# Performance work log

Measured on AMD Instinct MI355X. Metric: run time of the kernel, lower is better.

Reference implementation:

```python
import jax, jax.numpy as jnp
import numpy as np

D, H, KVH, HD, FF = 768, 12, 4, 64, 2048
N_REP = H // KVH
EPS = 1e-6


def rmsnorm(x, w):
    # Faithful to source: norm = ||x|| * n^{-1/2}; eps added to norm (not inside sqrt)
    norm = jnp.sqrt(jnp.sum(x * x, axis=-1, keepdims=True)) * (x.shape[-1] ** -0.5)
    return w * x / (norm + EPS)


def rope_tables(seq_len, head_dim, base=10000.0):
    inv_freq = 1.0 / (base ** (np.arange(0, head_dim, 2, dtype=np.float32) / head_dim))
    t = np.arange(seq_len, dtype=np.float32)
    freqs = np.einsum('i,j->ij', t, inv_freq)  # [S, HD/2]
    emb = np.concatenate([freqs, freqs], axis=-1)  # [S, HD]
    return jnp.asarray(np.cos(emb)), jnp.asarray(np.sin(emb))


def rotate_half(x):
    h = x.shape[-1] // 2
    return jnp.concatenate([-x[..., h:], x[..., :h]], axis=-1)


def setup_inputs() -> dict:
    key = jax.random.key(0)
    ks = jax.random.split(key, 9)
    s = 0.02
    return {
        'x': jax.random.normal(ks[0], (2, 2048, D), jnp.float32),
        'Wq': jax.random.normal(ks[1], (H * HD, D), jnp.float32) * s,
        'Wk': jax.random.normal(ks[2], (KVH * HD, D), jnp.float32) * s,
        'Wv': jax.random.normal(ks[3], (KVH * HD, D), jnp.float32) * s,
        'Wo': jax.random.normal(ks[4], (D, H * HD), jnp.float32) * s,
        'Wgate': jax.random.normal(ks[5], (FF, D), jnp.float32) * s,
        'Wup': jax.random.normal(ks[6], (FF, D), jnp.float32) * s,
        'Wdown': jax.random.normal(ks[7], (D, FF), jnp.float32) * s,
        'g1': jnp.ones((D,), jnp.float32),
        'g2': jnp.ones((D,), jnp.float32),
    }


def reference(x, Wq, Wk, Wv, Wo, Wgate, Wup, Wdown, g1, g2):
    B, S, _ = x.shape
    # ---- attention sublayer (pre-norm) ----
    xn = rmsnorm(x, g1)
    q = (xn @ Wq.T).reshape(B, S, H, HD).transpose(0, 2, 1, 3)      # [B,H,S,HD]
    k = (xn @ Wk.T).reshape(B, S, KVH, HD).transpose(0, 2, 1, 3)    # [B,KVH,S,HD]
    v = (xn @ Wv.T).reshape(B, S, KVH, HD).transpose(0, 2, 1, 3)
    cos, sin = rope_tables(S, HD)                                   # [S,HD]
    q = q * cos + rotate_half(q) * sin
    k = k * cos + rotate_half(k) * sin
    # repeat kv heads to match q heads
    k = jnp.repeat(k, N_REP, axis=1)                                # [B,H,S,HD]
    v = jnp.repeat(v, N_REP, axis=1)
    scores = jnp.einsum('bhqd,bhkd->bhqk', q, k) / jnp.sqrt(jnp.float32(HD))
    causal = jnp.tril(jnp.ones((S, S), bool))
    scores = jnp.where(causal, scores, jnp.finfo(scores.dtype).min)
    attn = jax.nn.softmax(scores, axis=-1)
    out = jnp.einsum('bhqk,bhkd->bhqd', attn, v)                    # [B,H,S,HD]
    out = out.transpose(0, 2, 1, 3).reshape(B, S, H * HD) @ Wo.T
    x = x + out
    # ---- SwiGLU FFN sublayer (pre-norm) ----
    xn2 = rmsnorm(x, g2)
    ff = (jax.nn.silu(xn2 @ Wgate.T) * (xn2 @ Wup.T)) @ Wdown.T
    return x + ff
```

## Files before the change

kernel.cpp:

```cpp
#include <hip/hip_runtime.h>
#include <hip/hip_bf16.h>
#include <math.h>

typedef __bf16 bf16;
typedef __attribute__((ext_vector_type(8))) __bf16 bf16x8;
typedef __attribute__((ext_vector_type(4))) __bf16 bf16x4;
typedef __attribute__((ext_vector_type(4))) float f32x4;

#define MFMA16(a,b,c) __builtin_amdgcn_mfma_f32_16x16x32_bf16(a,b,c,0,0,0)

#define BATCH 2
#define SEQ   2048
#define DMODEL 768
#define NH    12
#define NKV   4
#define NREP  3
#define HD    64
#define FFDIM 2048
#define ROWS  (BATCH*SEQ)

#define QSCALE 0.18033688011112042f
#define LOG2E  1.4426950408889634f

#define WB(N) asm volatile("s_waitcnt vmcnt(" #N ")\n\ts_barrier" ::: "memory")
#define BAR() asm volatile("s_barrier" ::: "memory")

__device__ __forceinline__ void gl2lds16(const bf16* g, bf16* l) {
  __builtin_amdgcn_global_load_lds(
      (const __attribute__((address_space(1))) void*)g,
      (__attribute__((address_space(3))) void*)l, 16, 0, 0);
}

#define SRC_SWZ(tt)  ((((tt) & 3) ^ (((tt) >> 3) & 3)) * 8)
#define RD_SWZ(l15,lq) (((lq) ^ (((l15) >> 1) & 3)) * 8)

struct Cvt7 { const float* s[7]; bf16* d[7]; int n[7]; };
__global__ __launch_bounds__(256) void cvt_all_kernel(Cvt7 c) {
  int seg = blockIdx.y;
  const float* __restrict__ src = c.s[seg];
  bf16* __restrict__ dst = c.d[seg];
  int n = c.n[seg];
  int stride = gridDim.x * 256;
  for (int i = blockIdx.x * 256 + threadIdx.x; i < n; i += stride)
    dst[i] = (bf16)src[i];
}

__global__ __launch_bounds__(256) void rope_tab_kernel(float* __restrict__ tab) {
  int id = blockIdx.x * 256 + threadIdx.x;
  int j = id >> 11, s = id & 2047;
  float inv = expf(-(float)j * (9.210340371976184f / 32.0f));
  float ang = (float)s * inv;
  tab[id] = cosf(ang);
  tab[65536 + id] = sinf(ang);
}

__global__ __launch_bounds__(192) void rmsnorm_kernel(const float* __restrict__ x,
    const float* __restrict__ g, bf16* __restrict__ out) {
  int row = blockIdx.x;
  const float* xr = x + (size_t)row * DMODEL;
  int t = threadIdx.x;
  f32x4 v = *(const f32x4*)(xr + t * 4);
  float ss = v[0] * v[0] + v[1] * v[1] + v[2] * v[2] + v[3] * v[3];
  #pragma unroll
  for (int off = 32; off; off >>= 1) ss += __shfl_xor(ss, off, 64);
  __shared__ float red[3];
  if ((t & 63) == 0) red[t >> 6] = ss;
  __syncthreads();
  float total = red[0] + red[1] + red[2];
  float norm = sqrtf(total) * 0.03608439182435161f;
  float sc = 1.0f / (norm + 1e-6f);
  f32x4 gv = *(const f32x4*)(g + t * 4);
  bf16x4 o;
  #pragma unroll
  for (int i = 0; i < 4; ++i) o[i] = (bf16)(gv[i] * v[i] * sc);
  *(bf16x4*)(out + (size_t)row * DMODEL + t * 4) = o;
}

__global__ __launch_bounds__(512, 6) void gemm_out_kernel(const bf16* __restrict__ A,
    const bf16* __restrict__ B, float* __restrict__ C, const float* __restrict__ R,
    int N, int K) {
  __shared__ __align__(16) bf16 At[2][3][64 * 32];
  __shared__ __align__(16) bf16 Bt[2][3][64 * 32];
  int t = threadIdx.x;
  int g = t >> 8;
  int tt = t & 255;
  int lane = t & 63;
  int w = (t >> 6) & 3;
  int l15 = lane & 15, lq = lane >> 4;
  int wrow = (w >> 1) * 32, wcol = (w & 1) * 32;
  int sw = RD_SWZ(l15, lq);

  int flat = blockIdx.y * 12 + blockIdx.x;
  int f2 = (flat & 7) * 96 + (flat >> 3);
  int col0 = (f2 % 12) * 64, row0 = (f2 / 12) * 64;

  const int KH = K >> 1;
  const int NS = KH / 32;
  int scol = SRC_SWZ(tt);
  const bf16* Ag = A + (size_t)(row0 + (tt >> 2)) * K + g * KH + scol;
  const bf16* Bg = B + (size_t)(col0 + (tt >> 2)) * K + g * KH + scol;

  #pragma unroll
  for (int s = 0; s < 3; ++s) {
    gl2lds16(Ag + s * 32, At[g][s] + tt * 8);
    gl2lds16(Bg + s * 32, Bt[g][s] + tt * 8);
  }

  f32x4 zero = {0.f, 0.f, 0.f, 0.f};
  f32x4 acc[2][2];
  #pragma unroll
  for (int m = 0; m < 2; ++m)
    #pragma unroll
    for (int n = 0; n < 2; ++n) acc[m][n] = zero;

  #define OG_COMPUTE(slot) do {                                              \
    const bf16* at = At[g][slot]; const bf16* bt = Bt[g][slot];              \
    bf16x8 af[2], bb[2];                                                     \
    _Pragma("unroll")                                                        \
    for (int m = 0; m < 2; ++m)                                              \
      af[m] = *(const bf16x8*)(at + (wrow + m * 16 + l15) * 32 + sw);        \
    _Pragma("unroll")                                                        \
    for (int n = 0; n < 2; ++n)                                              \
      bb[n] = *(const bf16x8*)(bt + (wcol + n * 16 + l15) * 32 + sw);        \
    _Pragma("unroll")                                                        \
    for (int m = 0; m < 2; ++m)                                              \
      _Pragma("unroll")                                                      \
      for (int n = 0; n < 2; ++n)                                            \
        acc[m][n] = MFMA16(af[m], bb[n], acc[m][n]);                         \
  } while (0)

  int slot = 0;
  for (int k = 0; k < NS - 2; ++k) {
    WB(4);
    OG_COMPUTE(slot);
    BAR();
    if (k <= NS - 4) {
      int ks = (k + 3) * 32;
      gl2lds16(Ag + ks, At[g][slot] + tt * 8);
      gl2lds16(Bg + ks, Bt[g][slot] + tt * 8);
    }
    slot = (slot == 2) ? 0 : slot + 1;
  }
  for (int k = NS - 2; k < NS; ++k) {
    WB(0);
    OG_COMPUTE(slot);
    slot = (slot == 2) ? 0 : slot + 1;
  }
  #undef OG_COMPUTE

  __syncthreads();
  float* Cl = (float*)&At[0][0][0];
  if (g == 1) {
    #pragma unroll
    for (int m = 0; m < 2; ++m)
      #pragma unroll
      for (int n = 0; n < 2; ++n)
        #pragma unroll
        for (int r = 0; r < 4; ++r)
          Cl[(wrow + m * 16 + lq * 4 + r) * 64 + wcol + n * 16 + l15] = acc[m][n][r];
  }
  __syncthreads();
  if (g == 0) {
    #pragma unroll
    for (int m = 0; m < 2; ++m)
      #pragma unroll
      for (int n = 0; n < 2; ++n)
        #pragma unroll
        for (int r = 0; r < 4; ++r) {
          int row = wrow + m * 16 + lq * 4 + r;
          int col = wcol + n * 16 + l15;
          size_t idx = (size_t)(row0 + row) * N + col0 + col;
          C[idx] = acc[m][n][r] + Cl[row * 64 + col] + R[idx];
        }
  }
}

__global__ __launch_bounds__(256) void gemm_qkv_kernel(const bf16* __restrict__ A,
    const bf16* __restrict__ Wcat, const float* __restrict__ tab,
    bf16* __restrict__ Qh, bf16* __restrict__ Kh, bf16* __restrict__ Vt) {
  __shared__ __align__(16) bf16 At[4][64 * 32];
  __shared__ __align__(16) bf16 Bt[4][128 * 32];
  const int K = DMODEL;
  int t = threadIdx.x, lane = t & 63, wave = t >> 6;
  int l15 = lane & 15, lq = lane >> 4;
  int wrow = (wave >> 1) * 32, wcol = (wave & 1) * 64;
  int sw = RD_SWZ(l15, lq);
  int row0 = blockIdx.y * 64, col0 = blockIdx.x * 128;
  int scol = SRC_SWZ(t);
  const bf16* Ag  = A + (size_t)(row0 + (t >> 2)) * K + scol;
  const bf16* Bg0 = Wcat + (size_t)(col0 + (t >> 2)) * K + scol;
  const bf16* Bg1 = Bg0 + (size_t)64 * K;
  const int NS = K / 32;

  #pragma unroll
  for (int s = 0; s < 4; ++s) {
    int ks = s * 32;
    gl2lds16(Ag + ks,  At[s] + t * 8);
    gl2lds16(Bg0 + ks, Bt[s] + t * 8);
    gl2lds16(Bg1 + ks, Bt[s] + 2048 + t * 8);
  }

  f32x4 zero = {0.f, 0.f, 0.f, 0.f};
  f32x4 acc[2][4];
  #pragma unroll
  for (int m = 0; m < 2; ++m)
    #pragma unroll
    for (int n = 0; n < 4; ++n) acc[m][n] = zero;

  #define QK_COMPUTE(slot) do {                                              \
    const bf16* at = At[slot]; const bf16* bt = Bt[slot];                    \
    bf16x8 af[2], bfr[4];                                                    \
    _Pragma("unroll")                                                        \
    for (int m = 0; m < 2; ++m)                                              \
      af[m] = *(const bf16x8*)(at + (wrow + m * 16 + l15) * 32 + sw);        \
    _Pragma("unroll")                                                        \
    for (int n = 0; n < 4; ++n)                                              \
      bfr[n] = *(const bf16x8*)(bt + (wcol + n * 16 + l15) * 32 + sw);       \
    _Pragma("unroll")                                                        \
    for (int m = 0; m < 2; ++m)                                              \
      _Pragma("unroll")                                                      \
      for (int n = 0; n < 4; ++n)                                            \
        acc[m][n] = MFMA16(af[m], bfr[n], acc[m][n]);                        \
  } while (0)

  for (int k = 0; k < NS - 3; ++k) {
    WB(9);
    QK_COMPUTE(k & 3);
    BAR();
    if (k <= NS - 5) {
      int ks = (k + 4) * 32;
      gl2lds16(Ag + ks,  At[k & 3] + t * 8);
      gl2lds16(Bg0 + ks, Bt[k & 3] + t * 8);
      gl2lds16(Bg1 + ks, Bt[k & 3] + 2048 + t * 8);
    }
  }
  for (int k = NS - 3; k < NS; ++k) {
    WB(0);
    QK_COMPUTE(k & 3);
  }
  #undef QK_COMPUTE

  int b = row0 >> 11;
  int s0 = (row0 & 2047) + wrow + lq * 4;
  int colw = col0 + wcol;
  if (colw < 768) {
    int h = colw >> 6;
    f32x4 cv[2][2], sv[2][2];
    #pragma unroll
    for (int m = 0; m < 2; ++m)
      #pragma unroll
      for (int jh = 0; jh < 2; ++jh) {
        const float* cp = tab + (jh * 16 + l15) * 2048 + s0 + m * 16;
        cv[m][jh] = *(const f32x4*)cp;
        sv[m][jh] = *(const f32x4*)(cp + 65536);
      }
    #pragma unroll
    for (int m = 0; m < 2; ++m)
      #pragma unroll
      for (int n = 0; n < 4; ++n) {
        float sgn = (n < 2) ? -1.f : 1.f;
        #pragma unroll
        for (int r = 0; r < 4; ++r) {
          float c = cv[m][n & 1][r], si = sv[m][n & 1][r];
          float rp = (acc[m][n][r] * c + sgn * acc[m][n ^ 2][r] * si) * QSCALE;
          Qh[((size_t)(b * NH + h) * SEQ + s0 + m * 16 + r) * 64 + n * 16 + l15] = (bf16)rp;
        }
      }
  } else if (colw < 1024) {
    int kh = (colw - 768) >> 6;
    f32x4 cv[2][2], sv[2][2];
    #pragma unroll
    for (int m = 0; m < 2; ++m)
      #pragma unroll
      for (int jh = 0; jh < 2; ++jh) {
        const float* cp = tab + (jh * 16 + l15) * 2048 + s0 + m * 16;
        cv[m][jh] = *(const f32x4*)cp;
        sv[m][jh] = *(const f32x4*)(cp + 65536);
      }
    #pragma unroll
    for (int m = 0; m < 2; ++m)
      #pragma unroll
      for (int n = 0; n < 4; ++n) {
        float sgn = (n < 2) ? -1.f : 1.f;
        #pragma unroll
        for (int r = 0; r < 4; ++r) {
          float c = cv[m][n & 1][r], si = sv[m][n & 1][r];
          float rp = acc[m][n][r] * c + sgn * acc[m][n ^ 2][r] * si;
          Kh[((size_t)(b * NKV + kh) * SEQ + s0 + m * 16 + r) * 64 + n * 16 + l15] = (bf16)rp;
        }
      }
  } else {
    int vh = (colw - 1024) >> 6;
    #pragma unroll
    for (int m = 0; m < 2; ++m)
      #pragma unroll
      for (int n = 0; n < 4; ++n) {
        bf16x4 pv;
        #pragma unroll
        for (int r = 0; r < 4; ++r) pv[r] = (bf16)acc[m][n][r];
        *(bf16x4*)(Vt + ((size_t)(b * NKV + vh) * 64 + n * 16 + l15) * SEQ + s0 + m * 16) = pv;
      }
  }
}

__global__ __launch_bounds__(256) void gemm_gu_kernel(const bf16* __restrict__ A,
    const bf16* __restrict__ Wg, const bf16* __restrict__ Wu, bf16* __restrict__ H) {
  __shared__ __align__(16) bf16 At[3][128 * 32];
  __shared__ __align__(16) bf16 Bgt[3][64 * 32];
  __shared__ __align__(16) bf16 But[3][64 * 32];
  const int K = DMODEL;
  int t = threadIdx.x, lane = t & 63, wave = t >> 6;
  int l15 = lane & 15, lq = lane >> 4;
  int wrow = (wave >> 1) * 64, wcol = (wave & 1) * 32;
  int sw = RD_SWZ(l15, lq);
  int row0 = blockIdx.y * 128, col0 = blockIdx.x * 64;
  int scol = SRC_SWZ(t);
  const bf16* Ag0 = A + (size_t)(row0 + (t >> 2)) * K + scol;
  const bf16* Ag1 = Ag0 + (size_t)64 * K;
  const bf16* Gg  = Wg + (size_t)(col0 + (t >> 2)) * K + scol;
  const bf16* Ug  = Wu + (size_t)(col0 + (t >> 2)) * K + scol;
  const int NS = K / 32;

  #pragma unroll
  for (int s = 0; s < 3; ++s) {
    int ks = s * 32;
    gl2lds16(Ag0 + ks, At[s] + t * 8);
    gl2lds16(Ag1 + ks, At[s] + 2048 + t * 8);
    gl2lds16(Gg + ks,  Bgt[s] + t * 8);
    gl2lds16(Ug + ks,  But[s] + t * 8);
  }

  f32x4 zero = {0.f, 0.f, 0.f, 0.f};
  f32x4 ag[4][2], au[4][2];
  #pragma unroll
  for (int m = 0; m < 4; ++m)
    #pragma unroll
    for (int n = 0; n < 2; ++n) { ag[m][n] = zero; au[m][n] = zero; }

  #define GU_COMPUTE(slot) do {                                              \
    const bf16* at = At[slot];                                               \
    const bf16* bgt = Bgt[slot]; const bf16* but = But[slot];                \
    bf16x8 af[4], bg[2], bu[2];                                              \
    _Pragma("unroll")                                                        \
    for (int m = 0; m < 4; ++m)                                              \
      af[m] = *(const bf16x8*)(at + (wrow + m * 16 + l15) * 32 + sw);        \
    _Pragma("unroll")                                                        \
    for (int n = 0; n < 2; ++n) {                                            \
      bg[n] = *(const bf16x8*)(bgt + (wcol + n * 16 + l15) * 32 + sw);       \
      bu[n] = *(const bf16x8*)(but + (wcol + n * 16 + l15) * 32 + sw);       \
    }                                                                        \
    _Pragma("unroll")                                                        \
    for (int m = 0; m < 4; ++m)                                              \
      _Pragma("unroll")                                                      \
      for (int n = 0; n < 2; ++n) {                                          \
        ag[m][n] = MFMA16(af[m], bg[n], ag[m][n]);                           \
        au[m][n] = MFMA16(af[m], bu[n], au[m][n]);                           \
      }                                                                      \
  } while (0)

  int slot = 0;
  for (int k = 0; k < NS - 2; ++k) {
    WB(8);
    GU_COMPUTE(slot);
    BAR();
    if (k <= NS - 4) {
      int ks = (k + 3) * 32;
      gl2lds16(Ag0 + ks, At[slot] + t * 8);
      gl2lds16(Ag1 + ks, At[slot] + 2048 + t * 8);
      gl2lds16(Gg + ks,  Bgt[slot] + t * 8);
      gl2lds16(Ug + ks,  But[slot] + t * 8);
    }
    slot = (slot == 2) ? 0 : slot + 1;
  }
  for (int k = NS - 2; k < NS; ++k) {
    WB(0);
    GU_COMPUTE(slot);
    slot = (slot == 2) ? 0 : slot + 1;
  }
  #undef GU_COMPUTE

  #pragma unroll
  for (int m = 0; m < 4; ++m)
    #pragma unroll
    for (int n = 0; n < 2; ++n)
      #pragma unroll
      for (int r = 0; r < 4; ++r) {
        int row = row0 + wrow + m * 16 + lq * 4 + r;
        int col = col0 + wcol + n * 16 + l15;
        float g = ag[m][n][r], u = au[m][n][r];
        float sg = g / (1.f + __builtin_amdgcn_exp2f(-g * LOG2E));
        H[(size_t)row * FFDIM + col] = (bf16)(sg * u);
      }
}

__global__ __launch_bounds__(256) void attn_kernel(const bf16* __restrict__ Qh,
    const bf16* __restrict__ Kh, const bf16* __restrict__ Vt, bf16* __restrict__ out) {
  __shared__ __align__(16) bf16 Kl0[2][64 * 32];
  __shared__ __align__(16) bf16 Kl1[2][64 * 32];
  __shared__ __align__(16) bf16 Vl0[2][64 * 32];
  __shared__ __align__(16) bf16 Vl1[2][64 * 32];
  __shared__ __align__(16) bf16 P[4][16 * 80];

  int idx = blockIdx.x;
  int qt = 31 - (idx / 24);
  int bh = idx % 24;
  int q0blk = qt * 64;
  int b = bh / NH, h = bh % NH;
  int kvh = h / NREP;
  int t = threadIdx.x;
  int lane = t & 63, wave = t >> 6;
  int l15 = lane & 15, lq = lane >> 4;
  int qw = q0blk + wave * 16;
  const bf16* Qb = Qh + (size_t)(b * NH + h) * SEQ * 64;
  const bf16* Kb = Kh + (size_t)(b * NKV + kvh) * SEQ * 64;
  const bf16* Vb = Vt + (size_t)(b * NKV + kvh) * 64 * SEQ;

  bf16x8 bq0 = *(const bf16x8*)(Qb + (size_t)(qw + l15) * 64 + lq * 8);
  bf16x8 bq1 = *(const bf16x8*)(Qb + (size_t)(qw + l15) * 64 + 32 + lq * 8);

  const bf16* Kg = Kb + (size_t)(t >> 2) * 64 + (t & 3) * 8;
  const bf16* Vg = Vb + (size_t)(t >> 2) * SEQ + (t & 3) * 8;
  bf16* Pw = P[wave];
  int Pwq = l15 * 80, lq8 = lq * 8, lq4 = lq * 4;
  const int NS = qt + 1;

  #pragma unroll
  for (int s = 0; s < 2; ++s) {
    int ks = (s < NS ? s : NS - 1) * 64;
    gl2lds16(Kg + (size_t)ks * 64,      Kl0[s] + t * 8);
    gl2lds16(Kg + (size_t)ks * 64 + 32, Kl1[s] + t * 8);
    gl2lds16(Vg + ks,                   Vl0[s] + t * 8);
    gl2lds16(Vg + ks + 32,              Vl1[s] + t * 8);
  }

  f32x4 zero = {0.f, 0.f, 0.f, 0.f};
  f32x4 o[4];
  o[0] = zero; o[1] = zero; o[2] = zero; o[3] = zero;
  float l_r = 0.f;

  #define ATTN_STEP(kk, slot) do {                                           \
    int k0 = (kk) * 64;                                                      \
    const bf16* kl0 = Kl0[slot]; const bf16* kl1 = Kl1[slot];                \
    const bf16* vl0 = Vl0[slot]; const bf16* vl1 = Vl1[slot];                \
    f32x4 s[4];                                                              \
    _Pragma("unroll")                                                        \
    for (int c = 0; c < 4; ++c) {                                            \
      bf16x8 ak0 = *(const bf16x8*)(kl0 + (c * 16 + l15) * 32 + lq8);        \
      bf16x8 ak1 = *(const bf16x8*)(kl1 + (c * 16 + l15) * 32 + lq8);        \
      s[c] = zero;                                                           \
      s[c] = MFMA16(ak0, bq0, s[c]);                                         \
      s[c] = MFMA16(ak1, bq1, s[c]);                                         \
    }                                                                        \
    if (k0 + 63 > qw) {                                                      \
      int qmk = qw + l15 - k0 - lq4;                                         \
      _Pragma("unroll")                                                      \
      for (int c = 0; c < 4; ++c)                                            \
        _Pragma("unroll")                                                    \
        for (int r = 0; r < 4; ++r)                                          \
          if (c * 16 + r > qmk) s[c][r] = -INFINITY;                         \
    }                                                                        \
    _Pragma("unroll")                                                        \
    for (int c = 0; c < 4; ++c) {                                            \
      bf16x4 pe;                                                             \
      _Pragma("unroll")                                                      \
      for (int r = 0; r < 4; ++r) {                                          \
        float e = __builtin_amdgcn_exp2f(s[c][r]);                           \
        l_r += e;                                                            \
        pe[r] = (bf16)e;                                                     \
      }                                                                      \
      *(bf16x4*)(Pw + Pwq + c * 16 + lq4) = pe;                              \
    }                                                                        \
    bf16x8 bp0 = *(const bf16x8*)(Pw + Pwq + lq8);                           \
    bf16x8 bp1 = *(const bf16x8*)(Pw + Pwq + 32 + lq8);                      \
    _Pragma("unroll")                                                        \
    for (int n = 0; n < 4; ++n) {                                            \
      bf16x8 av0 = *(const bf16x8*)(vl0 + (n * 16 + l15) * 32 + lq8);        \
      bf16x8 av1 = *(const bf16x8*)(vl1 + (n * 16 + l15) * 32 + lq8);        \
      o[n] = MFMA16(av0, bp0, o[n]);                                         \
      o[n] = MFMA16(av1, bp1, o[n]);                                         \
    }                                                                        \
  } while (0)

  for (int k = 0; k < NS - 1; ++k) {
    WB(4);
    ATTN_STEP(k, k & 1);
    BAR();
    if (k <= NS - 3) {
      int ks = (k + 2) * 64;
      gl2lds16(Kg + (size_t)ks * 64,      Kl0[k & 1] + t * 8);
      gl2lds16(Kg + (size_t)ks * 64 + 32, Kl1[k & 1] + t * 8);
      gl2lds16(Vg + ks,                   Vl0[k & 1] + t * 8);
      gl2lds16(Vg + ks + 32,              Vl1[k & 1] + t * 8);
    }
  }
  {
    WB(0);
    ATTN_STEP(NS - 1, (NS - 1) & 1);
  }
  #undef ATTN_STEP

  float lt = l_r;
  lt += __shfl_xor(lt, 16, 64);
  lt += __shfl_xor(lt, 32, 64);
  float inv = 1.f / lt;
  int q = qw + l15;
  bf16* orow = out + (size_t)(b * SEQ + q) * DMODEL + h * 64;
  #pragma unroll
  for (int n = 0; n < 4; ++n) {
    bf16x4 po;
    #pragma unroll
    for (int r = 0; r < 4; ++r) po[r] = (bf16)(o[n][r] * inv);
    *(bf16x4*)(orow + n * 16 + lq4) = po;
  }
}

extern "C" void kernel_launch(void* const* d_in, const int* in_sizes, int n_in,
                              void* d_out, int out_size, void* d_ws, size_t ws_size,
                              hipStream_t stream) {
  const float* x     = (const float*)d_in[0];
  const float* Wq    = (const float*)d_in[1];
  const float* Wk    = (const float*)d_in[2];
  const float* Wv    = (const float*)d_in[3];
  const float* Wo    = (const float*)d_in[4];
  const float* Wgate = (const float*)d_in[5];
  const float* Wup   = (const float*)d_in[6];
  const float* Wdown = (const float*)d_in[7];
  const float* g1    = (const float*)d_in[8];
  const float* g2    = (const float*)d_in[9];
  float* out = (float*)d_out;

  char* ws = (char*)d_ws;
  size_t off = 0;
  auto alloc = [&](size_t bytes) { size_t o = off; off += (bytes + 255) & ~(size_t)255; return o; };
  size_t o_tab  = alloc((size_t)2 * 32 * 2048 * 4);
  size_t o_x1   = alloc((size_t)4096 * 768 * 4);
  size_t o_xn   = alloc((size_t)4096 * 768 * 2);
  size_t o_Qh   = alloc((size_t)2 * 12 * 2048 * 64 * 2);
  size_t o_Kh   = alloc((size_t)2 * 4 * 2048 * 64 * 2);
  size_t o_Vt   = alloc((size_t)2 * 4 * 64 * 2048 * 2);
  size_t o_ao   = alloc((size_t)4096 * 768 * 2);
  size_t o_H    = alloc((size_t)4096 * 2048 * 2);
  size_t o_Wcat = alloc((size_t)1280 * 768 * 2);
  size_t o_Wo   = alloc((size_t)768 * 768 * 2);
  size_t o_Wgu  = alloc((size_t)4096 * 768 * 2);
  size_t o_Wdn  = alloc((size_t)768 * 2048 * 2);
  if (ws_size < off) return;

  float* tab  = (float*)(ws + o_tab);
  float* fx1  = (float*)(ws + o_x1);
  bf16* bxn   = (bf16*)(ws + o_xn);
  bf16* bQh   = (bf16*)(ws + o_Qh);
  bf16* bKh   = (bf16*)(ws + o_Kh);
  bf16* bVt   = (bf16*)(ws + o_Vt);
  bf16* bao   = (bf16*)(ws + o_ao);
  bf16* bH    = (bf16*)(ws + o_H);
  bf16* bWcat = (bf16*)(ws + o_Wcat);
  bf16* bWo   = (bf16*)(ws + o_Wo);
  bf16* bWgu  = (bf16*)(ws + o_Wgu);
  bf16* bWdn  = (bf16*)(ws + o_Wdn);

  rope_tab_kernel<<<256, 256, 0, stream>>>(tab);

  Cvt7 c;
  c.s[0] = Wq;    c.d[0] = bWcat;              c.n[0] = 768 * 768;
  c.s[1] = Wk;    c.d[1] = bWcat + 768 * 768;  c.n[1] = 256 * 768;
  c.s[2] = Wv;    c.d[2] = bWcat + 1024 * 768; c.n[2] = 256 * 768;
  c.s[3] = Wo;    c.d[3] = bWo;                c.n[3] = 768 * 768;
  c.s[4] = Wgate; c.d[4] = bWgu;               c.n[4] = 2048 * 768;
  c.s[5] = Wup;   c.d[5] = bWgu + 2048 * 768;  c.n[5] = 2048 * 768;
  c.s[6] = Wdown; c.d[6] = bWdn;               c.n[6] = 768 * 2048;
  cvt_all_kernel<<<dim3(256, 7), 256, 0, stream>>>(c);

  rmsnorm_kernel<<<4096, 192, 0, stream>>>(x, g1, bxn);
  gemm_qkv_kernel<<<dim3(10, 64), 256, 0, stream>>>(bxn, bWcat, tab, bQh, bKh, bVt);
  attn_kernel<<<dim3(768), 256, 0, stream>>>(bQh, bKh, bVt, bao);
  gemm_out_kernel<<<dim3(12, 64), 512, 0, stream>>>(bao, bWo, fx1, x, 768, 768);

  rmsnorm_kernel<<<4096, 192, 0, stream>>>(fx1, g2, bxn);
  gemm_gu_kernel<<<dim3(32, 32), 256, 0, stream>>>(bxn, bWgu, bWgu + 2048 * 768, bH);
  gemm_out_kernel<<<dim3(12, 64), 512, 0, stream>>>(bH, bWdn, out, fx1, 768, 2048);
}
```

Before: 245.8 us.

## Drop LDS swizzle and retile gate/up GEMM to 128x128 with 512 threads

Removes the XOR swizzle from the LDS staging layout in all GEMM kernels, using plain linear column offsets for both global-to-LDS loads and fragment reads. The gate/up GEMM grows from a 128x64 tile with 4 waves to a 128x128 tile with 8 waves, halving the grid and raising reuse of the A tile. The wait count is adjusted to match three loads per stage. Dropping the swizzle risks LDS bank conflicts on fragment reads, and the larger tile uses more LDS per block.

```diff
diff --git a/kernel.cpp b/kernel.cpp
--- a/kernel.cpp
+++ b/kernel.cpp
@@ -30,9 +30,6 @@
       (const __attribute__((address_space(1))) void*)g,
       (__attribute__((address_space(3))) void*)l, 16, 0, 0);
 }
-
-#define SRC_SWZ(tt)  ((((tt) & 3) ^ (((tt) >> 3) & 3)) * 8)
-#define RD_SWZ(l15,lq) (((lq) ^ (((l15) >> 1) & 3)) * 8)
 
 struct Cvt7 { const float* s[7]; bf16* d[7]; int n[7]; };
 __global__ __launch_bounds__(256) void cvt_all_kernel(Cvt7 c) {
@@ -88,7 +85,6 @@
   int w = (t >> 6) & 3;
   int l15 = lane & 15, lq = lane >> 4;
   int wrow = (w >> 1) * 32, wcol = (w & 1) * 32;
-  int sw = RD_SWZ(l15, lq);
 
   int flat = blockIdx.y * 12 + blockIdx.x;
   int f2 = (flat & 7) * 96 + (flat >> 3);
@@ -96,9 +92,8 @@
 
   const int KH = K >> 1;
   const int NS = KH / 32;
-  int scol = SRC_SWZ(tt);
-  const bf16* Ag = A + (size_t)(row0 + (tt >> 2)) * K + g * KH + scol;
-  const bf16* Bg = B + (size_t)(col0 + (tt >> 2)) * K + g * KH + scol;
+  const bf16* Ag = A + (size_t)(row0 + (tt >> 2)) * K + g * KH + (tt & 3) * 8;
+  const bf16* Bg = B + (size_t)(col0 + (tt >> 2)) * K + g * KH + (tt & 3) * 8;
 
   #pragma unroll
   for (int s = 0; s < 3; ++s) {
@@ -118,10 +113,10 @@
     bf16x8 af[2], bb[2];                                                     \
     _Pragma("unroll")                                                        \
     for (int m = 0; m < 2; ++m)                                              \
-      af[m] = *(const bf16x8*)(at + (wrow + m * 16 + l15) * 32 + sw);        \
+      af[m] = *(const bf16x8*)(at + (wrow + m * 16 + l15) * 32 + lq * 8);    \
     _Pragma("unroll")                                                        \
     for (int n = 0; n < 2; ++n)                                              \
-      bb[n] = *(const bf16x8*)(bt + (wcol + n * 16 + l15) * 32 + sw);        \
+      bb[n] = *(const bf16x8*)(bt + (wcol + n * 16 + l15) * 32 + lq * 8);    \
     _Pragma("unroll")                                                        \
     for (int m = 0; m < 2; ++m)                                              \
       _Pragma("unroll")                                                      \
@@ -184,11 +179,9 @@
   int t = threadIdx.x, lane = t & 63, wave = t >> 6;
   int l15 = lane & 15, lq = lane >> 4;
   int wrow = (wave >> 1) * 32, wcol = (wave & 1) * 64;
-  int sw = RD_SWZ(l15, lq);
   int row0 = blockIdx.y * 64, col0 = blockIdx.x * 128;
-  int scol = SRC_SWZ(t);
-  const bf16* Ag  = A + (size_t)(row0 + (t >> 2)) * K + scol;
-  const bf16* Bg0 = Wcat + (size_t)(col0 + (t >> 2)) * K + scol;
+  const bf16* Ag  = A + (size_t)(row0 + (t >> 2)) * K + (t & 3) * 8;
+  const bf16* Bg0 = Wcat + (size_t)(col0 + (t >> 2)) * K + (t & 3) * 8;
   const bf16* Bg1 = Bg0 + (size_t)64 * K;
   const int NS = K / 32;
 
@@ -212,10 +205,10 @@
     bf16x8 af[2], bfr[4];                                                    \
     _Pragma("unroll")                                                        \
     for (int m = 0; m < 2; ++m)                                              \
-      af[m] = *(const bf16x8*)(at + (wrow + m * 16 + l15) * 32 + sw);        \
+      af[m] = *(const bf16x8*)(at + (wrow + m * 16 + l15) * 32 + lq * 8);    \
     _Pragma("unroll")                                                        \
     for (int n = 0; n < 4; ++n)                                              \
-      bfr[n] = *(const bf16x8*)(bt + (wcol + n * 16 + l15) * 32 + sw);       \
+      bfr[n] = *(const bf16x8*)(bt + (wcol + n * 16 + l15) * 32 + lq * 8);   \
     _Pragma("unroll")                                                        \
     for (int m = 0; m < 2; ++m)                                              \
       _Pragma("unroll")                                                      \
@@ -303,31 +296,27 @@
   }
 }
 
-__global__ __launch_bounds__(256) void gemm_gu_kernel(const bf16* __restrict__ A,
+__global__ __launch_bounds__(512, 4) void gemm_gu_kernel(const bf16* __restrict__ A,
     const bf16* __restrict__ Wg, const bf16* __restrict__ Wu, bf16* __restrict__ H) {
   __shared__ __align__(16) bf16 At[3][128 * 32];
-  __shared__ __align__(16) bf16 Bgt[3][64 * 32];
-  __shared__ __align__(16) bf16 But[3][64 * 32];
+  __shared__ __align__(16) bf16 Bgt[3][128 * 32];
+  __shared__ __align__(16) bf16 But[3][128 * 32];
   const int K = DMODEL;
   int t = threadIdx.x, lane = t & 63, wave = t >> 6;
   int l15 = lane & 15, lq = lane >> 4;
-  int wrow = (wave >> 1) * 64, wcol = (wave & 1) * 32;
-  int sw = RD_SWZ(l15, lq);
-  int row0 = blockIdx.y * 128, col0 = blockIdx.x * 64;
-  int scol = SRC_SWZ(t);
-  const bf16* Ag0 = A + (size_t)(row0 + (t >> 2)) * K + scol;
-  const bf16* Ag1 = Ag0 + (size_t)64 * K;
-  const bf16* Gg  = Wg + (size_t)(col0 + (t >> 2)) * K + scol;
-  const bf16* Ug  = Wu + (size_t)(col0 + (t >> 2)) * K + scol;
+  int wrow = (wave >> 2) * 64, wcol = (wave & 3) * 32;
+  int row0 = blockIdx.y * 128, col0 = blockIdx.x * 128;
+  const bf16* Ag = A  + (size_t)(row0 + (t >> 2)) * K + (t & 3) * 8;
+  const bf16* Gg = Wg + (size_t)(col0 + (t >> 2)) * K + (t & 3) * 8;
+  const bf16* Ug = Wu + (size_t)(col0 + (t >> 2)) * K + (t & 3) * 8;
   const int NS = K / 32;
 
   #pragma unroll
   for (int s = 0; s < 3; ++s) {
     int ks = s * 32;
-    gl2lds16(Ag0 + ks, At[s] + t * 8);
-    gl2lds16(Ag1 + ks, At[s] + 2048 + t * 8);
-    gl2lds16(Gg + ks,  Bgt[s] + t * 8);
-    gl2lds16(Ug + ks,  But[s] + t * 8);
+    gl2lds16(Ag + ks, At[s] + t * 8);
+    gl2lds16(Gg + ks, Bgt[s] + t * 8);
+    gl2lds16(Ug + ks, But[s] + t * 8);
   }
 
   f32x4 zero = {0.f, 0.f, 0.f, 0.f};
@@ -343,11 +332,11 @@
     bf16x8 af[4], bg[2], bu[2];                                              \
     _Pragma("unroll")                                                        \
     for (int m = 0; m < 4; ++m)                                              \
-      af[m] = *(const bf16x8*)(at + (wrow + m * 16 + l15) * 32 + sw);        \
+      af[m] = *(const bf16x8*)(at + (wrow + m * 16 + l15) * 32 + lq * 8);    \
     _Pragma("unroll")                                                        \
     for (int n = 0; n < 2; ++n) {                                            \
-      bg[n] = *(const bf16x8*)(bgt + (wcol + n * 16 + l15) * 32 + sw);       \
-      bu[n] = *(const bf16x8*)(but + (wcol + n * 16 + l15) * 32 + sw);       \
+      bg[n] = *(const bf16x8*)(bgt + (wcol + n * 16 + l15) * 32 + lq * 8);   \
+      bu[n] = *(const bf16x8*)(but + (wcol + n * 16 + l15) * 32 + lq * 8);   \
     }                                                                        \
     _Pragma("unroll")                                                        \
     for (int m = 0; m < 4; ++m)                                              \
@@ -360,15 +349,14 @@
 
   int slot = 0;
   for (int k = 0; k < NS - 2; ++k) {
-    WB(8);
+    WB(6);
     GU_COMPUTE(slot);
     BAR();
     if (k <= NS - 4) {
       int ks = (k + 3) * 32;
-      gl2lds16(Ag0 + ks, At[slot] + t * 8);
-      gl2lds16(Ag1 + ks, At[slot] + 2048 + t * 8);
-      gl2lds16(Gg + ks,  Bgt[slot] + t * 8);
-      gl2lds16(Ug + ks,  But[slot] + t * 8);
+      gl2lds16(Ag + ks, At[slot] + t * 8);
+      gl2lds16(Gg + ks, Bgt[slot] + t * 8);
+      gl2lds16(Ug + ks, But[slot] + t * 8);
     }
     slot = (slot == 2) ? 0 : slot + 1;
   }
@@ -577,6 +565,6 @@
   gemm_out_kernel<<<dim3(12, 64), 512, 0, stream>>>(bao, bWo, fx1, x, 768, 768);
 
   rmsnorm_kernel<<<4096, 192, 0, stream>>>(fx1, g2, bxn);
-  gemm_gu_kernel<<<dim3(32, 32), 256, 0, stream>>>(bxn, bWgu, bWgu + 2048 * 768, bH);
+  gemm_gu_kernel<<<dim3(16, 32), 512, 0, stream>>>(bxn, bWgu, bWgu + 2048 * 768, bH);
   gemm_out_kernel<<<dim3(12, 64), 512, 0, stream>>>(bH, bWdn, out, fx1, 768, 2048);
 }
```

After: 246.5 us. Within noise of the previous version (+0.3%).
